# Kernel tuning notes

Hardware: AMD Instinct MI355X
Metric: run time of the kernel (lower is better)

## Reference

```python
import jax, jax.numpy as jnp
import numpy as np

NEG_INF = -1e30


def setup_inputs() -> dict:
    B, N, D = 512, 256, 256
    key = jax.random.key(0)
    ks = jax.random.split(key, 10)
    s = 1.0 / np.sqrt(D)
    return {
        "enc": jax.random.normal(ks[0], (B, N, D), dtype=jnp.float32),
        "init_token": jax.random.normal(ks[1], (D,), dtype=jnp.float32),
        "w_ih": jax.random.uniform(ks[2], (3 * D, D), minval=-s, maxval=s, dtype=jnp.float32),
        "w_hh": jax.random.uniform(ks[3], (3 * D, D), minval=-s, maxval=s, dtype=jnp.float32),
        "b_ih": jax.random.uniform(ks[4], (3 * D,), minval=-s, maxval=s, dtype=jnp.float32),
        "b_hh": jax.random.uniform(ks[5], (3 * D,), minval=-s, maxval=s, dtype=jnp.float32),
        "wq": jax.random.uniform(ks[6], (D, D), minval=-s, maxval=s, dtype=jnp.float32),
        "bq": jax.random.uniform(ks[7], (D,), minval=-s, maxval=s, dtype=jnp.float32),
        "wk": jax.random.uniform(ks[8], (D, D), minval=-s, maxval=s, dtype=jnp.float32),
        "bk": jax.random.uniform(ks[9], (D,), minval=-s, maxval=s, dtype=jnp.float32),
    }


def gru_cell(x, h, w_ih, w_hh, b_ih, b_hh):
    # torch.nn.GRUCell math; gates packed as [reset, update, new]
    gi = x @ w_ih.T + b_ih          # [B, 3D]
    gh = h @ w_hh.T + b_hh          # [B, 3D]
    D = h.shape[-1]
    i_r, i_z, i_n = gi[:, :D], gi[:, D:2 * D], gi[:, 2 * D:]
    h_r, h_z, h_n = gh[:, :D], gh[:, D:2 * D], gh[:, 2 * D:]
    r = jax.nn.sigmoid(i_r + h_r)
    z = jax.nn.sigmoid(i_z + h_z)
    n = jnp.tanh(i_n + r * h_n)
    return (1.0 - z) * n + z * h


def pointer_decode(enc, init_token, w_ih, w_hh, b_ih, b_hh, wq, bq, wk, bk):
    # Greedy decode (deterministic analogue of decode_type='greedy').
    B, N, D = enc.shape
    scale = 1.0 / np.sqrt(D)
    keys = enc @ wk.T + bk                         # [B, N, D]
    rows = jnp.arange(B)

    def step(carry, _):
        state, prev_embed, mask = carry
        state = gru_cell(prev_embed, state, w_ih, w_hh, b_ih, b_hh)   # [B, D]
        query = state @ wq.T + bq                                     # [B, D]
        logits = jnp.einsum('bd,bnd->bn', query, keys) * scale        # [B, N]
        logits = jnp.where(mask, logits, NEG_INF)
        logp = jax.nn.log_softmax(logits, axis=-1)                    # [B, N]
        probs = jnp.exp(logp)
        entropy = -jnp.sum(probs * jnp.where(mask, logp, 0.0), axis=-1)  # [B]
        idx = jnp.argmax(probs, axis=-1)                              # [B]
        step_logp = logp[rows, idx]                                   # [B]
        prev_embed = enc[rows, idx]                                   # [B, D]
        mask = mask.at[rows, idx].set(False)
        return (state, prev_embed, mask), (idx, step_logp, entropy)

    carry0 = (enc.mean(axis=1),
              jnp.broadcast_to(init_token, (B, D)),
              jnp.ones((B, N), dtype=bool))
    _, (tours, logps, ents) = jax.lax.scan(step, carry0, None, length=N)
    return tours.T, logps.T, ents.T  # each [B, N]


def reference(enc, init_token, w_ih, w_hh, b_ih, b_hh, wq, bq, wk, bk):
    return pointer_decode(enc, init_token, w_ih, w_hh, b_ih, b_hh, wq, bq, wk, bk)
```

## Files before the change

### kernel.cpp

```cpp
#include <hip/hip_runtime.h>

#define B_ 512
#define N_ 256
#define D_ 256
#define NEGINF (-1e30)

#define PD(c) ((c) + ((c) >> 6))

typedef float v4f __attribute__((ext_vector_type(4)));

__device__ __forceinline__ v4f ntload4(const v4f* p) {
  return __builtin_nontemporal_load(p);
}

__global__ __launch_bounds__(256) void packW_k(const float* __restrict__ in,
                                               float* __restrict__ out) {
  int idx = blockIdx.x * 256 + threadIdx.x;
  int j = idx >> 6, c4 = idx & 63;
  int g = j >> 8, o = j & 255;
  int w16 = o >> 4, k = c4 & 15, l = 4 * (o & 15) + (c4 >> 4);
  ((v4f*)out)[((w16 * 16 + k) * 3 + g) * 64 + l] = ((const v4f*)in)[idx];
}

__global__ __launch_bounds__(256) void wqk_k(const float* __restrict__ wk,
                                             const float* __restrict__ wq,
                                             const float* __restrict__ bq,
                                             double* __restrict__ WqkP,
                                             double* __restrict__ bqk) {
  int c = blockIdx.x, e = threadIdx.x;
  double acc = 0.0;
  for (int dd = 0; dd < 256; ++dd)
    acc += (double)wk[dd * 256 + c] * (double)wq[dd * 256 + e];
  int w16 = c >> 4, k2 = (e >> 1) & 31, l = 4 * (c & 15) + (e >> 6), comp = e & 1;
  WqkP[(size_t)(((w16 * 32) + k2) * 64 + l) * 2 + comp] = acc;
  if (e == 0) {
    double s = 0.0;
    for (int dd = 0; dd < 256; ++dd) s += (double)wk[dd * 256 + c] * (double)bq[dd];
    bqk[c] = s;
  }
}

__global__ __launch_bounds__(256) void encp_k(const float* __restrict__ enc,
                                              float* __restrict__ encP) {
  int b = blockIdx.y;
  int idx = blockIdx.x * 256 + threadIdx.x;
  int l = idx & 63, rest = idx >> 6;
  int k = rest & 15, w16 = rest >> 4;
  int n = w16 * 16 + (l >> 2), c4 = (l & 3) * 16 + k;
  ((v4f*)encP)[(size_t)b * 16384 + idx] =
      *(const v4f*)(enc + (size_t)b * 65536 + n * 256 + c4 * 4);
}

__global__ __launch_bounds__(1024, 4) void decode_k(
    const float* __restrict__ enc, const float* __restrict__ init_token,
    const float* __restrict__ b_ih, const float* __restrict__ b_hh,
    const float* __restrict__ wihP, const float* __restrict__ whhP,
    const double* __restrict__ WqkP, const double* __restrict__ bqk,
    const float* __restrict__ encP, float* __restrict__ out) {
  const int tid = threadIdx.x;
  const int WV = tid >> 6;
  const int LN = tid & 63;
  const int O = WV * 16 + (LN >> 2);
  const int S = LN & 3;
  const int ROW = S >> 1;
  const int b0 = blockIdx.x * 2;

  __shared__ alignas(16) double hS[2][2][260];
  __shared__ alignas(16) double xS[2][260];
  __shared__ alignas(16) double qs[2][260];
  __shared__ double lg[2][N_];
  __shared__ unsigned char maskS[2][N_];
  __shared__ double redA[16][2], redB[16][2], redC[16][2];
  __shared__ int redI[16][2];

  const float* encB0 = enc + (size_t)b0 * 65536;
  const float* encB1 = encB0 + 65536;
  const v4f* eP0 = (const v4f*)encP + (size_t)b0 * 16384;
  const v4f* eP1 = eP0 + 16384;
  const v4f* wh4 = (const v4f*)whhP;
  const v4f* wi4 = (const v4f*)wihP;
  const double2* Wp2 = (const double2*)WqkP;

  if (tid < 256) {
    double iv = (double)init_token[tid];
    xS[0][PD(tid)] = iv;
    xS[1][PD(tid)] = iv;
    maskS[0][tid] = 1;
    maskS[1][tid] = 1;
  }
  {
    double p0 = 0.0, p1 = 0.0;
    const float* e0 = encB0 + (size_t)(S * 64) * 256 + O;
    const float* e1 = encB1 + (size_t)(S * 64) * 256 + O;
#pragma unroll 4
    for (int n = 0; n < 64; ++n) { p0 += (double)e0[n * 256]; p1 += (double)e1[n * 256]; }
    p0 += __shfl_xor(p0, 1); p0 += __shfl_xor(p0, 2);
    p1 += __shfl_xor(p1, 1); p1 += __shfl_xor(p1, 2);
    if (S == 0) {
      hS[0][0][PD(O)] = p0 * (1.0 / 256.0);
      hS[0][1][PD(O)] = p1 * (1.0 / 256.0);
    }
  }
  __syncthreads();

  int cur = 0;
  for (int t = 0; t < N_; ++t) {
    const int nxt = cur ^ 1;
    double ghr0 = 0, ghz0 = 0, ghn0 = 0, ghr1 = 0, ghz1 = 0, ghn1 = 0;
    double air0 = 0, aiz0 = 0, ain0 = 0, air1 = 0, aiz1 = 0, ain1 = 0;
#pragma unroll 4
    for (int k = 0; k < 16; ++k) {
      int wb = ((WV * 16 + k) * 3) * 64 + LN;
      v4f br = wh4[wb], bz = wh4[wb + 64], bn = wh4[wb + 128];
      v4f ar = wi4[wb], az = wi4[wb + 64], an = wi4[wb + 128];
      int c = S * 64 + 4 * k;
      const double* h0 = &hS[cur][0][c + S];
      const double* h1 = &hS[cur][1][c + S];
      const double* x0 = &xS[0][c + S];
      const double* x1 = &xS[1][c + S];
#pragma unroll
      for (int i = 0; i < 4; ++i) {
        double wr = (double)br[i], wz = (double)bz[i], wn = (double)bn[i];
        ghr0 += wr * h0[i]; ghz0 += wz * h0[i]; ghn0 += wn * h0[i];
        ghr1 += wr * h1[i]; ghz1 += wz * h1[i]; ghn1 += wn * h1[i];
        double vr = (double)ar[i], vz = (double)az[i], vn = (double)an[i];
        air0 += vr * x0[i]; aiz0 += vz * x0[i]; ain0 += vn * x0[i];
        air1 += vr * x1[i]; aiz1 += vz * x1[i]; ain1 += vn * x1[i];
      }
    }
    ghr0 += __shfl_xor(ghr0, 1); ghr0 += __shfl_xor(ghr0, 2);
    ghz0 += __shfl_xor(ghz0, 1); ghz0 += __shfl_xor(ghz0, 2);
    ghn0 += __shfl_xor(ghn0, 1); ghn0 += __shfl_xor(ghn0, 2);
    ghr1 += __shfl_xor(ghr1, 1); ghr1 += __shfl_xor(ghr1, 2);
    ghz1 += __shfl_xor(ghz1, 1); ghz1 += __shfl_xor(ghz1, 2);
    ghn1 += __shfl_xor(ghn1, 1); ghn1 += __shfl_xor(ghn1, 2);
    air0 += __shfl_xor(air0, 1); air0 += __shfl_xor(air0, 2);
    aiz0 += __shfl_xor(aiz0, 1); aiz0 += __shfl_xor(aiz0, 2);
    ain0 += __shfl_xor(ain0, 1); ain0 += __shfl_xor(ain0, 2);
    air1 += __shfl_xor(air1, 1); air1 += __shfl_xor(air1, 2);
    aiz1 += __shfl_xor(aiz1, 1); aiz1 += __shfl_xor(aiz1, 2);
    ain1 += __shfl_xor(ain1, 1); ain1 += __shfl_xor(ain1, 2);
    {
      double gir = (ROW ? air1 : air0) + (double)b_ih[O];
      double giz = (ROW ? aiz1 : aiz0) + (double)b_ih[256 + O];
      double gin = (ROW ? ain1 : ain0) + (double)b_ih[512 + O];
      double hr_ = (ROW ? ghr1 : ghr0) + (double)b_hh[O];
      double hz_ = (ROW ? ghz1 : ghz0) + (double)b_hh[256 + O];
      double hn_ = (ROW ? ghn1 : ghn0) + (double)b_hh[512 + O];
      double rr = 1.0 / (1.0 + exp(-(gir + hr_)));
      double zz = 1.0 / (1.0 + exp(-(giz + hz_)));
      double nn = tanh(gin + rr * hn_);
      double hold = hS[cur][ROW][PD(O)];
      double hnew = (1.0 - zz) * nn + zz * hold;
      if ((S & 1) == 0) hS[nxt][ROW][PD(O)] = hnew;
    }
    __syncthreads();

    {
      double q0 = 0, q1 = 0;
#pragma unroll 4
      for (int k = 0; k < 32; ++k) {
        double2 wv = Wp2[(WV * 32 + k) * 64 + LN];
        int dd = S * 64 + 2 * k;
        const double* h0 = &hS[nxt][0][dd + S];
        const double* h1 = &hS[nxt][1][dd + S];
        q0 += wv.x * h0[0] + wv.y * h0[1];
        q1 += wv.x * h1[0] + wv.y * h1[1];
      }
      q0 += __shfl_xor(q0, 1); q0 += __shfl_xor(q0, 2);
      q1 += __shfl_xor(q1, 1); q1 += __shfl_xor(q1, 2);
      if (S == 0) {
        double bb = bqk[O];
        qs[0][PD(O)] = q0 + bb;
        qs[1][PD(O)] = q1 + bb;
      }
    }
    __syncthreads();

    double lgv0, lgv1;
    {
      double p0 = 0, p1 = 0;
#pragma unroll 2
      for (int k = 0; k < 16; ++k) {
        int eb = (WV * 16 + k) * 64 + LN;
        v4f e0 = ntload4(eP0 + eb);
        v4f e1 = ntload4(eP1 + eb);
        int c = S * 64 + 4 * k;
        const double* qa = &qs[0][c + S];
        const double* qb = &qs[1][c + S];
#pragma unroll
        for (int i = 0; i < 4; ++i) {
          p0 += (double)e0[i] * qa[i];
          p1 += (double)e1[i] * qb[i];
        }
      }
      p0 += __shfl_xor(p0, 1); p0 += __shfl_xor(p0, 2);
      p1 += __shfl_xor(p1, 1); p1 += __shfl_xor(p1, 2);
      lgv0 = 0.0625 * p0; if (!maskS[0][O]) lgv0 = NEGINF;
      lgv1 = 0.0625 * p1; if (!maskS[1][O]) lgv1 = NEGINF;
      if (S == 0) { lg[0][O] = lgv0; lg[1][O] = lgv1; }
      double v0 = lgv0, v1 = lgv1;
      int i0 = O, i1 = O;
#pragma unroll
      for (int off = 1; off < 64; off <<= 1) {
        double t0 = __shfl_xor(v0, off); int ti0 = __shfl_xor(i0, off);
        if (t0 > v0 || (t0 == v0 && ti0 < i0)) { v0 = t0; i0 = ti0; }
        double t1 = __shfl_xor(v1, off); int ti1 = __shfl_xor(i1, off);
        if (t1 > v1 || (t1 == v1 && ti1 < i1)) { v1 = t1; i1 = ti1; }
      }
      if (LN == 0) { redA[WV][0] = v0; redI[WV][0] = i0; redA[WV][1] = v1; redI[WV][1] = i1; }
    }
    __syncthreads();

    double m0 = -1e300, m1 = -1e300;
    int am0 = 0, am1 = 0;
#pragma unroll 4
    for (int w = 0; w < 16; ++w) {
      double va = redA[w][0]; int ia = redI[w][0];
      if (va > m0 || (va == m0 && ia < am0)) { m0 = va; am0 = ia; }
      double vb = redA[w][1]; int ib = redI[w][1];
      if (vb > m1 || (vb == m1 && ib < am1)) { m1 = vb; am1 = ib; }
    }
    {
      double e0 = (S == 0) ? exp(lgv0 - m0) : 0.0;
      double e1 = (S == 0) ? exp(lgv1 - m1) : 0.0;
      double s20 = e0 * (lgv0 - m0);
      double s21 = e1 * (lgv1 - m1);
#pragma unroll
      for (int off = 1; off < 64; off <<= 1) {
        e0 += __shfl_xor(e0, off);
        e1 += __shfl_xor(e1, off);
        s20 += __shfl_xor(s20, off);
        s21 += __shfl_xor(s21, off);
      }
      if (LN == 0) { redB[WV][0] = e0; redB[WV][1] = e1; redC[WV][0] = s20; redC[WV][1] = s21; }
    }
    if (tid < 512) {
      int r = tid >> 8, j = tid & 255;
      int am = r ? am1 : am0;
      int c4 = j >> 2;
      int vidx = ((am >> 4) * 16 + (c4 & 15)) * 64 + (4 * (am & 15) + (c4 >> 4));
      const float* ePr = r ? (const float*)eP1 : (const float*)eP0;
      xS[r][PD(j)] = (double)__builtin_nontemporal_load(ePr + vidx * 4 + (j & 3));
    }
    __syncthreads();

    if (tid < 2) {
      int r = tid;
      double m = r ? m1 : m0;
      int am = r ? am1 : am0;
      double S1 = 0, S2 = 0;
#pragma unroll 4
      for (int w = 0; w < 16; ++w) { S1 += redB[w][r]; S2 += redC[w][r]; }
      double lS = log(S1);
      double logZ = m + lS;
      size_t row = (size_t)(b0 + r) * N_;
      out[row + t] = (float)am;
      out[(size_t)B_ * N_ + row + t] = (float)(lg[r][am] - logZ);
      out[2 * (size_t)B_ * N_ + row + t] = (float)(lS - S2 / S1);
      maskS[r][am] = 0;
    }
    __syncthreads();
    cur ^= 1;
  }
}

extern "C" void kernel_launch(void* const* d_in, const int* in_sizes, int n_in,
                              void* d_out, int out_size, void* d_ws, size_t ws_size,
                              hipStream_t stream) {
  const float* enc = (const float*)d_in[0];
  const float* init_token = (const float*)d_in[1];
  const float* w_ih = (const float*)d_in[2];
  const float* w_hh = (const float*)d_in[3];
  const float* b_ih = (const float*)d_in[4];
  const float* b_hh = (const float*)d_in[5];
  const float* wq = (const float*)d_in[6];
  const float* bq = (const float*)d_in[7];
  const float* wk = (const float*)d_in[8];
  const float* bk = (const float*)d_in[9];
  (void)bk;
  float* out = (float*)d_out;
  char* wsb = (char*)d_ws;

  float* wihP = (float*)(wsb + 0);
  float* whhP = (float*)(wsb + 786432);
  double* WqkP = (double*)(wsb + 1572864);
  double* bqk = (double*)(wsb + 2097152);
  float* encP = (float*)(wsb + 2099200);

  hipLaunchKernelGGL(packW_k, dim3(192), dim3(256), 0, stream, w_ih, wihP);
  hipLaunchKernelGGL(packW_k, dim3(192), dim3(256), 0, stream, w_hh, whhP);
  hipLaunchKernelGGL(wqk_k, dim3(256), dim3(256), 0, stream, wk, wq, bq, WqkP, bqk);
  hipLaunchKernelGGL(encp_k, dim3(64, 512), dim3(256), 0, stream, enc, encP);
  hipLaunchKernelGGL(decode_k, dim3(B_ / 2), dim3(1024), 0, stream, enc, init_token,
                     b_ih, b_hh, wihP, whhP, WqkP, bqk, encP, out);
}
```

Before: 17.23 ms.

## Use online-softmax per-wave partials to drop a barrier per decode step

Each wave now computes its local max and rescaled exp/entropy partial sums in one pass. A 32-lane shuffle merge then combines them with log-sum-exp rescaling, which removes one __syncthreads and the serial tid<2 reduction from every step. The shared-memory padding changes from 1 to 2 doubles per 64 (stride 66) to reduce LDS bank conflicts. Unroll factors go up and the nontemporal loads become plain loads so the hot enc tile can stay in cache. The trade-off is extra exp work per wave and a redundant 16-way argmax by the 512 gather threads.

```diff
diff --git a/kernel.cpp b/kernel.cpp
--- a/kernel.cpp
+++ b/kernel.cpp
@@ -5,13 +5,7 @@
 #define D_ 256
 #define NEGINF (-1e30)
 
-#define PD(c) ((c) + ((c) >> 6))
-
 typedef float v4f __attribute__((ext_vector_type(4)));
-
-__device__ __forceinline__ v4f ntload4(const v4f* p) {
-  return __builtin_nontemporal_load(p);
-}
 
 __global__ __launch_bounds__(256) void packW_k(const float* __restrict__ in,
                                                float* __restrict__ out) {
@@ -64,10 +58,12 @@
   const int S = LN & 3;
   const int ROW = S >> 1;
   const int b0 = blockIdx.x * 2;
-
-  __shared__ alignas(16) double hS[2][2][260];
-  __shared__ alignas(16) double xS[2][260];
-  __shared__ alignas(16) double qs[2][260];
+  const int OP = O + ((O >> 6) << 1);
+  const int CB = S * 66;
+
+  __shared__ alignas(16) double hS[2][2][264];
+  __shared__ alignas(16) double xS[2][264];
+  __shared__ alignas(16) double qs[2][264];
   __shared__ double lg[2][N_];
   __shared__ unsigned char maskS[2][N_];
   __shared__ double redA[16][2], redB[16][2], redC[16][2];
@@ -83,8 +79,9 @@
 
   if (tid < 256) {
     double iv = (double)init_token[tid];
-    xS[0][PD(tid)] = iv;
-    xS[1][PD(tid)] = iv;
+    int p = tid + ((tid >> 6) << 1);
+    xS[0][p] = iv;
+    xS[1][p] = iv;
     maskS[0][tid] = 1;
     maskS[1][tid] = 1;
   }
@@ -97,8 +94,8 @@
     p0 += __shfl_xor(p0, 1); p0 += __shfl_xor(p0, 2);
     p1 += __shfl_xor(p1, 1); p1 += __shfl_xor(p1, 2);
     if (S == 0) {
-      hS[0][0][PD(O)] = p0 * (1.0 / 256.0);
-      hS[0][1][PD(O)] = p1 * (1.0 / 256.0);
+      hS[0][0][OP] = p0 * (1.0 / 256.0);
+      hS[0][1][OP] = p1 * (1.0 / 256.0);
     }
   }
   __syncthreads();
@@ -113,11 +110,10 @@
       int wb = ((WV * 16 + k) * 3) * 64 + LN;
       v4f br = wh4[wb], bz = wh4[wb + 64], bn = wh4[wb + 128];
       v4f ar = wi4[wb], az = wi4[wb + 64], an = wi4[wb + 128];
-      int c = S * 64 + 4 * k;
-      const double* h0 = &hS[cur][0][c + S];
-      const double* h1 = &hS[cur][1][c + S];
-      const double* x0 = &xS[0][c + S];
-      const double* x1 = &xS[1][c + S];
+      const double* h0 = &hS[cur][0][CB + 4 * k];
+      const double* h1 = &hS[cur][1][CB + 4 * k];
+      const double* x0 = &xS[0][CB + 4 * k];
+      const double* x1 = &xS[1][CB + 4 * k];
 #pragma unroll
       for (int i = 0; i < 4; ++i) {
         double wr = (double)br[i], wz = (double)bz[i], wn = (double)bn[i];
@@ -150,20 +146,19 @@
       double rr = 1.0 / (1.0 + exp(-(gir + hr_)));
       double zz = 1.0 / (1.0 + exp(-(giz + hz_)));
       double nn = tanh(gin + rr * hn_);
-      double hold = hS[cur][ROW][PD(O)];
+      double hold = hS[cur][ROW][OP];
       double hnew = (1.0 - zz) * nn + zz * hold;
-      if ((S & 1) == 0) hS[nxt][ROW][PD(O)] = hnew;
+      if ((S & 1) == 0) hS[nxt][ROW][OP] = hnew;
     }
     __syncthreads();
 
     {
       double q0 = 0, q1 = 0;
-#pragma unroll 4
+#pragma unroll 8
       for (int k = 0; k < 32; ++k) {
         double2 wv = Wp2[(WV * 32 + k) * 64 + LN];
-        int dd = S * 64 + 2 * k;
-        const double* h0 = &hS[nxt][0][dd + S];
-        const double* h1 = &hS[nxt][1][dd + S];
+        const double* h0 = &hS[nxt][0][CB + 2 * k];
+        const double* h1 = &hS[nxt][1][CB + 2 * k];
         q0 += wv.x * h0[0] + wv.y * h0[1];
         q1 += wv.x * h1[0] + wv.y * h1[1];
       }
@@ -171,23 +166,21 @@
       q1 += __shfl_xor(q1, 1); q1 += __shfl_xor(q1, 2);
       if (S == 0) {
         double bb = bqk[O];
-        qs[0][PD(O)] = q0 + bb;
-        qs[1][PD(O)] = q1 + bb;
+        qs[0][OP] = q0 + bb;
+        qs[1][OP] = q1 + bb;
       }
     }
     __syncthreads();
 
-    double lgv0, lgv1;
     {
       double p0 = 0, p1 = 0;
-#pragma unroll 2
+#pragma unroll 8
       for (int k = 0; k < 16; ++k) {
         int eb = (WV * 16 + k) * 64 + LN;
-        v4f e0 = ntload4(eP0 + eb);
-        v4f e1 = ntload4(eP1 + eb);
-        int c = S * 64 + 4 * k;
-        const double* qa = &qs[0][c + S];
-        const double* qb = &qs[1][c + S];
+        v4f e0 = eP0[eb];
+        v4f e1 = eP1[eb];
+        const double* qa = &qs[0][CB + 4 * k];
+        const double* qb = &qs[1][CB + 4 * k];
 #pragma unroll
         for (int i = 0; i < 4; ++i) {
           p0 += (double)e0[i] * qa[i];
@@ -196,8 +189,8 @@
       }
       p0 += __shfl_xor(p0, 1); p0 += __shfl_xor(p0, 2);
       p1 += __shfl_xor(p1, 1); p1 += __shfl_xor(p1, 2);
-      lgv0 = 0.0625 * p0; if (!maskS[0][O]) lgv0 = NEGINF;
-      lgv1 = 0.0625 * p1; if (!maskS[1][O]) lgv1 = NEGINF;
+      double lgv0 = 0.0625 * p0; if (!maskS[0][O]) lgv0 = NEGINF;
+      double lgv1 = 0.0625 * p1; if (!maskS[1][O]) lgv1 = NEGINF;
       if (S == 0) { lg[0][O] = lgv0; lg[1][O] = lgv1; }
       double v0 = lgv0, v1 = lgv1;
       int i0 = O, i1 = O;
@@ -208,57 +201,67 @@
         double t1 = __shfl_xor(v1, off); int ti1 = __shfl_xor(i1, off);
         if (t1 > v1 || (t1 == v1 && ti1 < i1)) { v1 = t1; i1 = ti1; }
       }
-      if (LN == 0) { redA[WV][0] = v0; redI[WV][0] = i0; redA[WV][1] = v1; redI[WV][1] = i1; }
-    }
-    __syncthreads();
-
-    double m0 = -1e300, m1 = -1e300;
-    int am0 = 0, am1 = 0;
-#pragma unroll 4
-    for (int w = 0; w < 16; ++w) {
-      double va = redA[w][0]; int ia = redI[w][0];
-      if (va > m0 || (va == m0 && ia < am0)) { m0 = va; am0 = ia; }
-      double vb = redA[w][1]; int ib = redI[w][1];
-      if (vb > m1 || (vb == m1 && ib < am1)) { m1 = vb; am1 = ib; }
-    }
-    {
-      double e0 = (S == 0) ? exp(lgv0 - m0) : 0.0;
-      double e1 = (S == 0) ? exp(lgv1 - m1) : 0.0;
-      double s20 = e0 * (lgv0 - m0);
-      double s21 = e1 * (lgv1 - m1);
+      double e0 = (S == 0) ? exp(lgv0 - v0) : 0.0;
+      double e1 = (S == 0) ? exp(lgv1 - v1) : 0.0;
+      double s20 = e0 * (lgv0 - v0);
+      double s21 = e1 * (lgv1 - v1);
 #pragma unroll
       for (int off = 1; off < 64; off <<= 1) {
         e0 += __shfl_xor(e0, off);
+        s20 += __shfl_xor(s20, off);
         e1 += __shfl_xor(e1, off);
-        s20 += __shfl_xor(s20, off);
         s21 += __shfl_xor(s21, off);
       }
-      if (LN == 0) { redB[WV][0] = e0; redB[WV][1] = e1; redC[WV][0] = s20; redC[WV][1] = s21; }
+      if (LN == 0) {
+        redA[WV][0] = v0; redI[WV][0] = i0; redB[WV][0] = e0; redC[WV][0] = s20;
+        redA[WV][1] = v1; redI[WV][1] = i1; redB[WV][1] = e1; redC[WV][1] = s21;
+      }
+    }
+    __syncthreads();
+
+    if (tid < 32) {
+      int r = LN >> 4, w = LN & 15;
+      double mw = redA[w][r];
+      int iw = redI[w][r];
+      double s1w = redB[w][r], s2w = redC[w][r];
+      double m = mw;
+      int am = iw;
+#pragma unroll
+      for (int off = 1; off < 16; off <<= 1) {
+        double om = __shfl_xor(m, off); int oi = __shfl_xor(am, off);
+        if (om > m || (om == m && oi < am)) { m = om; am = oi; }
+      }
+      double sc = exp(mw - m);
+      double S1 = s1w * sc;
+      double S2 = (s2w + (mw - m) * s1w) * sc;
+#pragma unroll
+      for (int off = 1; off < 16; off <<= 1) {
+        S1 += __shfl_xor(S1, off);
+        S2 += __shfl_xor(S2, off);
+      }
+      if (w == 0) {
+        double lS = log(S1);
+        double logZ = m + lS;
+        size_t row = (size_t)(b0 + r) * N_;
+        out[row + t] = (float)am;
+        out[(size_t)B_ * N_ + row + t] = (float)(lg[r][am] - logZ);
+        out[2 * (size_t)B_ * N_ + row + t] = (float)(lS - S2 / S1);
+        maskS[r][am] = 0;
+      }
     }
     if (tid < 512) {
       int r = tid >> 8, j = tid & 255;
-      int am = r ? am1 : am0;
+      double bv = redA[0][r];
+      int am = redI[0][r];
+#pragma unroll 4
+      for (int w = 1; w < 16; ++w) {
+        double wv = redA[w][r]; int wi = redI[w][r];
+        if (wv > bv || (wv == bv && wi < am)) { bv = wv; am = wi; }
+      }
       int c4 = j >> 2;
       int vidx = ((am >> 4) * 16 + (c4 & 15)) * 64 + (4 * (am & 15) + (c4 >> 4));
       const float* ePr = r ? (const float*)eP1 : (const float*)eP0;
-      xS[r][PD(j)] = (double)__builtin_nontemporal_load(ePr + vidx * 4 + (j & 3));
-    }
-    __syncthreads();
-
-    if (tid < 2) {
-      int r = tid;
-      double m = r ? m1 : m0;
-      int am = r ? am1 : am0;
-      double S1 = 0, S2 = 0;
-#pragma unroll 4
-      for (int w = 0; w < 16; ++w) { S1 += redB[w][r]; S2 += redC[w][r]; }
-      double lS = log(S1);
-      double logZ = m + lS;
-      size_t row = (size_t)(b0 + r) * N_;
-      out[row + t] = (float)am;
-      out[(size_t)B_ * N_ + row + t] = (float)(lg[r][am] - logZ);
-      out[2 * (size_t)B_ * N_ + row + t] = (float)(lS - S2 / S1);
-      maskS[r][am] = 0;
+      xS[r][j + ((j >> 6) << 1)] = (double)ePr[vidx * 4 + (j & 3)];
     }
     __syncthreads();
     cur ^= 1;
```

Measured after the change: 19.06 ms. 10.6% more time.
